# Kernel tuning notes

Hardware: AMD Instinct MI355X
Metric: run time of the kernel (lower is better)

The kernel has to match this reference:

```python
import jax, jax.numpy as jnp
import numpy as np

FACTOR = 5


def setup_inputs() -> dict:
    key = jax.random.key(0)
    k1, k2, k3, k4 = jax.random.split(key, 4)
    B, L, H, D = 4, 2048, 8, 64
    sample_k = min(FACTOR * int(np.ceil(np.log(L))), L)  # 40
    return {
        "query": jax.random.normal(k1, (B, L, H, D), dtype=jnp.float32),
        "key": jax.random.normal(k2, (B, L, H, D), dtype=jnp.float32),
        "value": jax.random.normal(k3, (B, L, H, D), dtype=jnp.float32),
        "index_sample": jax.random.randint(k4, (L, sample_k), 0, L, dtype=jnp.int32),
    }


def reference(query, key, value, index_sample):
    # query/key/value: (B, L, H, D); mask_flag=True, output_attention=False
    B, L_Q, H, D = query.shape
    L_K = key.shape[1]
    q = jnp.swapaxes(query, 1, 2)  # (B,H,L_Q,D)
    k = jnp.swapaxes(key, 1, 2)    # (B,H,L_K,D)
    v = jnp.swapaxes(value, 1, 2)  # (B,H,L_K,D)

    U_part = min(FACTOR * int(np.ceil(np.log(L_K))), L_K)  # sample_k
    u = min(FACTOR * int(np.ceil(np.log(L_Q))), L_Q)       # n_top

    # --- _prob_QK: sampled QK scores, sparsity measure M, top-u queries ---
    # K_sample: gather sample_k keys per query position -> (B,H,L_Q,sample_k,D)
    K_sample = k[:, :, index_sample, :]
    Q_K_sample = jnp.einsum("bhid,bhisd->bhis", q, K_sample)  # (B,H,L_Q,sample_k)
    M = Q_K_sample.max(axis=-1) - Q_K_sample.sum(axis=-1) / L_K  # (B,H,L_Q)
    _, M_top = jax.lax.top_k(M, u)  # (B,H,u) indices of selected queries

    Q_reduce = jnp.take_along_axis(q, M_top[..., None], axis=2)  # (B,H,u,D)
    scores = jnp.einsum("bhud,bhkd->bhuk", Q_reduce, k)          # (B,H,u,L_K)

    scale = 1.0 / jnp.sqrt(jnp.float32(D))
    scores = scores * scale

    # --- initial context: causal cumsum of V (mask_flag=True) ---
    context = jnp.cumsum(v, axis=2)  # (B,H,L_Q,D)

    # --- update context: causal ProbMask on selected rows, softmax, scatter ---
    # mask[b,h,t,kk] = kk > M_top[b,h,t]
    mask = jnp.arange(L_K)[None, None, None, :] > M_top[..., None]
    scores = jnp.where(mask, -jnp.inf, scores)
    attn = jax.nn.softmax(scores, axis=-1)
    ctx_upd = jnp.einsum("bhuk,bhkd->bhud", attn, v)  # (B,H,u,D)

    b_idx = jnp.arange(context.shape[0])[:, None, None]
    h_idx = jnp.arange(context.shape[1])[None, :, None]
    context = context.at[b_idx, h_idx, M_top].set(ctx_upd)

    return jnp.swapaxes(context, 1, 2)  # (B, L_Q, H, D)
```

## Files before the change

kernel.cpp:

```cpp
#include <hip/hip_runtime.h>
#include <hip/hip_bf16.h>
#include <math.h>

constexpr int B = 4;
constexpr int L = 2048;
constexpr int H = 8;
constexpr int D = 64;
constexpr int S = 40;
constexpr int U = 40;
constexpr int C = 32;
constexpr int CHUNK = L / C;
constexpr int NSEG = 16;
constexpr int SEG  = L / NSEG;
constexpr int PAH  = 688;

__global__ void fused_Mpart(const float* __restrict__ q,
                            const float* __restrict__ k,
                            const float* __restrict__ v,
                            const int*   __restrict__ samp,
                            float* __restrict__ M,
                            float* __restrict__ part) {
    __shared__ float pa[H * PAH];
    int tid = threadIdx.x;

    if (blockIdx.x < 256) {
        int idx = blockIdx.x * 256 + tid;
        int b   = idx >> 14;
        int rem = idx & 16383;
        int c   = rem >> 9;
        int hd  = rem & 511;
        const float* base = v + ((size_t)(b * L + c * CHUNK) * H * D) + hd;
        float s = 0.f;
        for (int i = 0; i < CHUNK; i++) s += base[(size_t)i * (H * D)];
        int h = hd >> 6, d = hd & 63;
        part[((size_t)(b * H + h) * C + c) * D + d] = s;
        return;
    }

    int blk = blockIdx.x - 256;
    int xcd = blk & 7;
    int b   = xcd >> 1;
    int l   = ((blk >> 3) << 1) | (xcd & 1);
    int h      = tid >> 5;
    int lane32 = tid & 31;
    int g  = lane32 >> 4;
    int d4 = lane32 & 15;

    const float4 qv = *(const float4*)(q + ((size_t)(b * L + l) * H + h) * D + d4 * 4);
    const int* srow = samp + l * S;
    float* pah = pa + h * PAH;

#pragma unroll 10
    for (int sb = 0; sb < S; sb += 2) {
        int i0 = srow[sb];
        int i1 = srow[sb + 1];
        int idx = g ? i1 : i0;
        int s = sb + g;
        float4 kv = *(const float4*)(k + ((size_t)(b * L + idx) * H + h) * D + d4 * 4);
        pah[s * 17 + d4] = qv.x * kv.x + qv.y * kv.y + qv.z * kv.z + qv.w * kv.w;
    }
    __syncthreads();

    int s1 = lane32;
    float t0 = 0.f, t1 = 0.f, t2 = 0.f, t3 = 0.f;
#pragma unroll
    for (int i = 0; i < 16; i += 4) {
        t0 += pah[s1 * 17 + i];
        t1 += pah[s1 * 17 + i + 1];
        t2 += pah[s1 * 17 + i + 2];
        t3 += pah[s1 * 17 + i + 3];
    }
    float dot1 = (t0 + t1) + (t2 + t3);
    float mv = dot1, sv = dot1;
    if (lane32 < S - 32) {
        int s2 = 32 + lane32;
        float u0 = 0.f, u1 = 0.f, u2 = 0.f, u3 = 0.f;
#pragma unroll
        for (int i = 0; i < 16; i += 4) {
            u0 += pah[s2 * 17 + i];
            u1 += pah[s2 * 17 + i + 1];
            u2 += pah[s2 * 17 + i + 2];
            u3 += pah[s2 * 17 + i + 3];
        }
        float dot2 = (u0 + u1) + (u2 + u3);
        mv = fmaxf(mv, dot2);
        sv += dot2;
    }
#pragma unroll
    for (int off = 1; off <= 16; off <<= 1) {
        mv = fmaxf(mv, __shfl_xor(mv, off));
        sv += __shfl_xor(sv, off);
    }
    if (lane32 == 0) M[(size_t)(b * H + h) * L + l] = mv - sv * (1.0f / (float)L);
}

__global__ void fused_topk_cumsum(const float* __restrict__ M,
                                  const float* __restrict__ v,
                                  const float* __restrict__ part,
                                  int* __restrict__ Mtop,
                                  float* __restrict__ out) {
    int tid = threadIdx.x;

    if (blockIdx.x >= 32) {
        int idx = (blockIdx.x - 32) * 64 + tid;
        int b   = idx >> 14;
        int rem = idx & 16383;
        int c   = rem >> 9;
        int hd  = rem & 511;
        int h = hd >> 6, d = hd & 63;

        float run = 0.f;
        for (int cc = 0; cc < c; cc++)
            run += part[((size_t)(b * H + h) * C + cc) * D + d];

        const float* base  = v   + ((size_t)(b * L + c * CHUNK) * H * D) + hd;
        float*       obase = out + ((size_t)(b * L + c * CHUNK) * H * D) + hd;
        for (int i = 0; i < CHUNK; i++) {
            run += base[(size_t)i * (H * D)];
            obase[(size_t)i * (H * D)] = run;
        }
        return;
    }

    int bh   = blockIdx.x;
    int base = tid * 32;
    const float* row = M + (size_t)bh * L;

    unsigned int vals[32];
#pragma unroll
    for (int r4 = 0; r4 < 8; r4++) {
        float4 f = *(const float4*)(row + base + r4 * 4);
        const float ff[4] = {f.x, f.y, f.z, f.w};
#pragma unroll
        for (int j = 0; j < 4; j++) {
            unsigned int i = __float_as_uint(ff[j]);
            vals[r4 * 4 + j] = (i & 0x80000000u) ? ~i : (i | 0x80000000u);
        }
    }

    unsigned long long k1 = 0ull, k2 = 0ull;
#pragma unroll
    for (int r = 0; r < 32; r++) {
        unsigned long long kk =
            ((unsigned long long)vals[r] << 32) | (unsigned int)~(base + r);
        if (kk > k1) { k2 = k1; k1 = kk; }
        else if (kk > k2) { k2 = kk; }
    }

    for (int it = 0; it < U; it += 2) {
        unsigned long long a1 = k1, a2 = k2;
#pragma unroll
        for (int off = 1; off < 64; off <<= 1) {
            unsigned long long o1 = __shfl_xor(a1, off);
            unsigned long long o2 = __shfl_xor(a2, off);
            unsigned long long hi = a1 > o1 ? a1 : o1;
            unsigned long long lo = a1 > o1 ? o1 : a1;
            unsigned long long ss = a2 > o2 ? a2 : o2;
            a1 = hi;
            a2 = lo > ss ? lo : ss;
        }
        int i1 = (int)~(unsigned int)a1;
        int i2 = (int)~(unsigned int)a2;
        if (tid == 0) {
            Mtop[bh * U + it]     = i1;
            Mtop[bh * U + it + 1] = i2;
        }
        bool own1 = (i1 >> 5) == tid;
        bool own2 = (i2 >> 5) == tid;
        if (own1 | own2) {
            int r1 = own1 ? (i1 & 31) : 32;
            int r2 = own2 ? (i2 & 31) : 32;
#pragma unroll
            for (int r = 0; r < 32; r++)
                if (r == r1 || r == r2) vals[r] = 0u;
            k1 = 0ull; k2 = 0ull;
#pragma unroll
            for (int r = 0; r < 32; r++) {
                unsigned long long kk =
                    ((unsigned long long)vals[r] << 32) | (unsigned int)~(base + r);
                if (kk > k1) { k2 = k1; k1 = kk; }
                else if (kk > k2) { k2 = kk; }
            }
        }
    }
}

__global__ __launch_bounds__(256, 2)
void attn_batched(const float* __restrict__ q,
                  const float* __restrict__ k,
                  const float* __restrict__ v,
                  const int*   __restrict__ Mtop,
                  float* __restrict__ ml,
                  float* __restrict__ pacc) {
    int blk = blockIdx.x;
    int xcd = blk & 7;
    int b   = xcd >> 1;
    int r   = ((blk >> 3) << 1) | (xcd & 1);
    int h   = r >> 4;
    int seg = r & 15;
    int bh  = b * H + h;
    int j0  = seg * SEG;
    int tid = threadIdx.x;

    __shared__ float Qs[U * D];
    __shared__ float KV[SEG * D];
    __shared__ float Sc[U * SEG];
    __shared__ float red[U * 4];
    __shared__ float mrow[U];
    __shared__ int   qis[U];

    if (tid < U) qis[tid] = Mtop[bh * U + tid];
    __syncthreads();

    for (int i = tid; i < U * 16; i += 256) {
        int u = i >> 4, d4 = i & 15;
        *(float4*)&Qs[u * D + d4 * 4] =
            *(const float4*)(q + ((size_t)(b * L + qis[u]) * H + h) * D + d4 * 4);
    }
    for (int i = tid; i < SEG * 16; i += 256) {
        int rr = i >> 4, d4 = i & 15;
        float4 kv = *(const float4*)(k + ((size_t)(b * L + j0 + rr) * H + h) * D + d4 * 4);
        *(float4*)&KV[rr * D + (d4 ^ (rr & 15)) * 4] = kv;
    }
    __syncthreads();

    int ug = tid >> 5;
    int jg = tid & 31;
    int jlow = jg & 15;
    float acc[5][4];
#pragma unroll
    for (int uu = 0; uu < 5; uu++)
#pragma unroll
        for (int jj = 0; jj < 4; jj++) acc[uu][jj] = 0.f;

#pragma unroll
    for (int kk4 = 0; kk4 < 16; kk4++) {
        float4 kf[4];
        int slot = kk4 ^ jlow;
#pragma unroll
        for (int jj = 0; jj < 4; jj++)
            kf[jj] = *(const float4*)&KV[(jg + 32 * jj) * D + slot * 4];
#pragma unroll
        for (int uu = 0; uu < 5; uu++) {
            float4 qf = *(const float4*)&Qs[(ug * 5 + uu) * D + kk4 * 4];
#pragma unroll
            for (int jj = 0; jj < 4; jj++) {
                acc[uu][jj] += qf.x * kf[jj].x + qf.y * kf[jj].y
                             + qf.z * kf[jj].z + qf.w * kf[jj].w;
            }
        }
    }
#pragma unroll
    for (int uu = 0; uu < 5; uu++) {
        int u = ug * 5 + uu;
        int um = u & 15;
#pragma unroll
        for (int jj = 0; jj < 4; jj++) {
            int j = jg + 32 * jj;
            Sc[u * SEG + 4 * ((j >> 2) ^ um) + (j & 3)] = acc[uu][jj] * 0.125f;
        }
    }
    __syncthreads();

    for (int i = tid; i < SEG * 16; i += 256) {
        int rr = i >> 4, d4 = i & 15;
        float4 vv = *(const float4*)(v + ((size_t)(b * L + j0 + rr) * H + h) * D + d4 * 4);
        *(float4*)&KV[rr * D + (d4 ^ (rr & 15)) * 4] = vv;
    }

    int su = tid >> 2, sq = tid & 3;
    int nkc = 0;
    if (tid < U * 4) {
        int nk = qis[su] + 1 - j0;
        nkc = nk < 0 ? 0 : (nk > SEG ? SEG : nk);
        int um = su & 15;
        float mvx = -INFINITY;
        for (int t = 0; t < 32; t++) {
            int i = sq + 4 * t;
            if (i < nkc) mvx = fmaxf(mvx, Sc[su * SEG + 4 * ((i >> 2) ^ um) + (i & 3)]);
        }
        red[su * 4 + sq] = mvx;
    }
    __syncthreads();
    if (tid < U) {
        float m = fmaxf(fmaxf(red[tid * 4], red[tid * 4 + 1]),
                        fmaxf(red[tid * 4 + 2], red[tid * 4 + 3]));
        mrow[tid] = m;
    }
    __syncthreads();
    if (tid < U * 4) {
        float m = mrow[su];
        int um = su & 15;
        float ls = 0.f;
        for (int t = 0; t < 32; t++) {
            int i = sq + 4 * t;
            int addr = su * SEG + 4 * ((i >> 2) ^ um) + (i & 3);
            float e = 0.f;
            if (i < nkc) e = __expf(Sc[addr] - m);
            Sc[addr] = e;
            ls += e;
        }
        red[su * 4 + sq] = ls;
    }
    __syncthreads();
    if (tid < U) {
        float ls = (red[tid * 4] + red[tid * 4 + 1]) + (red[tid * 4 + 2] + red[tid * 4 + 3]);
        size_t mli = 2 * ((size_t)(bh * U + tid) * NSEG + seg);
        ml[mli]     = mrow[tid];
        ml[mli + 1] = ls;
    }

    int vg = jg;
    float a2[5][2];
#pragma unroll
    for (int uu = 0; uu < 5; uu++) { a2[uu][0] = 0.f; a2[uu][1] = 0.f; }

    for (int j4 = 0; j4 < 32; j4++) {
        float4 pf[5];
#pragma unroll
        for (int uu = 0; uu < 5; uu++) {
            int u = ug * 5 + uu;
            pf[uu] = *(const float4*)&Sc[u * SEG + 4 * (j4 ^ (u & 15))];
        }
#pragma unroll
        for (int jj = 0; jj < 4; jj++) {
            int j = j4 * 4 + jj;
            int fo = 4 * ((vg >> 1) ^ (j & 15)) + ((2 * vg) & 3);
            float2 vv = *(const float2*)&KV[j * D + fo];
#pragma unroll
            for (int uu = 0; uu < 5; uu++) {
                float p = ((const float*)&pf[uu])[jj];
                a2[uu][0] += p * vv.x;
                a2[uu][1] += p * vv.y;
            }
        }
    }
#pragma unroll
    for (int uu = 0; uu < 5; uu++) {
        int u = ug * 5 + uu;
        float2 w2 = make_float2(a2[uu][0], a2[uu][1]);
        *(float2*)&pacc[((size_t)(bh * U + u) * NSEG + seg) * D + 2 * vg] = w2;
    }
}

__global__ void attn_combine(const int* __restrict__ Mtop,
                             const float* __restrict__ ml,
                             const float* __restrict__ pacc,
                             float* __restrict__ out) {
    int row = blockIdx.x * 4 + (threadIdx.x >> 6);
    int u  = row % U;
    int bh = row / U;
    int h  = bh % H;
    int b  = bh / H;
    int d  = threadIdx.x & 63;
    int qi = Mtop[bh * U + u];

    size_t r0 = (size_t)row * NSEG;
    float m = -INFINITY;
#pragma unroll
    for (int s = 0; s < NSEG; s++) m = fmaxf(m, ml[2 * (r0 + s)]);

    float lt = 0.f, acc = 0.f;
#pragma unroll
    for (int s = 0; s < NSEG; s++) {
        float ms = ml[2 * (r0 + s)];
        float w  = __expf(ms - m);
        lt  += ml[2 * (r0 + s) + 1] * w;
        acc += pacc[(r0 + s) * D + d] * w;
    }
    out[((size_t)(b * L + qi) * H + h) * D + d] = acc / lt;
}

extern "C" void kernel_launch(void* const* d_in, const int* in_sizes, int n_in,
                              void* d_out, int out_size, void* d_ws, size_t ws_size,
                              hipStream_t stream) {
    const float* q    = (const float*)d_in[0];
    const float* k    = (const float*)d_in[1];
    const float* v    = (const float*)d_in[2];
    const int*   samp = (const int*)d_in[3];
    float* out = (float*)d_out;

    float* M    = (float*)d_ws;
    int*   Mtop = (int*)(M + (size_t)B * H * L);
    float* part = (float*)(Mtop + (size_t)B * H * U);
    float* ml   = part + (size_t)B * H * C * D;
    float* pacc = ml + (size_t)B * H * U * NSEG * 2;

    fused_Mpart<<<256 + B * L, 256, 0, stream>>>(q, k, v, samp, M, part);
    fused_topk_cumsum<<<32 + 1024, 64, 0, stream>>>(M, v, part, Mtop, out);
    attn_batched<<<B * H * NSEG, 256, 0, stream>>>(q, k, v, Mtop, ml, pacc);
    attn_combine<<<B * H * U / 4, 256, 0, stream>>>(Mtop, ml, pacc, out);
}
```

Baseline: 184.4 us.

## Replace iterative warp top-k with radix-select histogram threshold and compaction

```diff
diff --git a/kernel.cpp b/kernel.cpp
--- a/kernel.cpp
+++ b/kernel.cpp
@@ -122,65 +122,106 @@
         return;
     }
 
+    __shared__ unsigned hist[16 * 256];
+    __shared__ unsigned selS[2];
+
     int bh   = blockIdx.x;
-    int base = tid * 32;
+    int lane = tid;
+    int base = lane * 32;
     const float* row = M + (size_t)bh * L;
 
-    unsigned int vals[32];
+    unsigned vals[32];
 #pragma unroll
     for (int r4 = 0; r4 < 8; r4++) {
         float4 f = *(const float4*)(row + base + r4 * 4);
         const float ff[4] = {f.x, f.y, f.z, f.w};
 #pragma unroll
         for (int j = 0; j < 4; j++) {
-            unsigned int i = __float_as_uint(ff[j]);
+            unsigned i = __float_as_uint(ff[j]);
             vals[r4 * 4 + j] = (i & 0x80000000u) ? ~i : (i | 0x80000000u);
         }
     }
 
-    unsigned long long k1 = 0ull, k2 = 0ull;
+    unsigned prefix = 0;
+    unsigned R = U;
+#pragma unroll
+    for (int p = 0; p < 4; p++) {
+        int sh = 24 - 8 * p;
+        {
+            uint4* h4 = (uint4*)hist;
+#pragma unroll
+            for (int i = 0; i < 16; i++) {
+                h4[lane + i * 64] = make_uint4(0u, 0u, 0u, 0u);
+            }
+        }
+        __syncthreads();
+        unsigned pbase = (lane & 15) * 256;
+#pragma unroll
+        for (int r = 0; r < 32; r++) {
+            unsigned vv = vals[r];
+            bool match = (p == 0) || ((vv >> (sh + 8)) == prefix);
+            if (match) atomicAdd(&hist[pbase + ((vv >> sh) & 255u)], 1u);
+        }
+        __syncthreads();
+        int b0 = lane * 4;
+        unsigned c0 = 0, c1 = 0, c2 = 0, c3 = 0;
+#pragma unroll
+        for (int pp = 0; pp < 16; pp++) {
+            const unsigned* hp = &hist[pp * 256 + b0];
+            c0 += hp[0]; c1 += hp[1]; c2 += hp[2]; c3 += hp[3];
+        }
+        unsigned t = c0 + c1 + c2 + c3;
+        unsigned s = t;
+#pragma unroll
+        for (int off = 1; off < 64; off <<= 1) {
+            unsigned n = __shfl_down(s, off);
+            if (lane + off < 64) s += n;
+        }
+        unsigned Sx = s - t;
+        unsigned suf3 = Sx;
+        unsigned suf2 = Sx + c3;
+        unsigned suf1 = Sx + c3 + c2;
+        unsigned suf0 = Sx + c3 + c2 + c1;
+        if (suf0 < R && R <= suf0 + c0) { selS[0] = b0;     selS[1] = R - suf0; }
+        if (suf1 < R && R <= suf1 + c1) { selS[0] = b0 + 1; selS[1] = R - suf1; }
+        if (suf2 < R && R <= suf2 + c2) { selS[0] = b0 + 2; selS[1] = R - suf2; }
+        if (suf3 < R && R <= suf3 + c3) { selS[0] = b0 + 3; selS[1] = R - suf3; }
+        __syncthreads();
+        prefix = (prefix << 8) | selS[0];
+        R = selS[1];
+        __syncthreads();
+    }
+    unsigned vstar = prefix;
+    unsigned Rstar = R;
+    unsigned n1 = U - Rstar;
+
+    unsigned cgt = 0, ceq = 0;
 #pragma unroll
     for (int r = 0; r < 32; r++) {
-        unsigned long long kk =
-            ((unsigned long long)vals[r] << 32) | (unsigned int)~(base + r);
-        if (kk > k1) { k2 = k1; k1 = kk; }
-        else if (kk > k2) { k2 = kk; }
-    }
-
-    for (int it = 0; it < U; it += 2) {
-        unsigned long long a1 = k1, a2 = k2;
-#pragma unroll
-        for (int off = 1; off < 64; off <<= 1) {
-            unsigned long long o1 = __shfl_xor(a1, off);
-            unsigned long long o2 = __shfl_xor(a2, off);
-            unsigned long long hi = a1 > o1 ? a1 : o1;
-            unsigned long long lo = a1 > o1 ? o1 : a1;
-            unsigned long long ss = a2 > o2 ? a2 : o2;
-            a1 = hi;
-            a2 = lo > ss ? lo : ss;
-        }
-        int i1 = (int)~(unsigned int)a1;
-        int i2 = (int)~(unsigned int)a2;
-        if (tid == 0) {
-            Mtop[bh * U + it]     = i1;
-            Mtop[bh * U + it + 1] = i2;
-        }
-        bool own1 = (i1 >> 5) == tid;
-        bool own2 = (i2 >> 5) == tid;
-        if (own1 | own2) {
-            int r1 = own1 ? (i1 & 31) : 32;
-            int r2 = own2 ? (i2 & 31) : 32;
-#pragma unroll
-            for (int r = 0; r < 32; r++)
-                if (r == r1 || r == r2) vals[r] = 0u;
-            k1 = 0ull; k2 = 0ull;
-#pragma unroll
-            for (int r = 0; r < 32; r++) {
-                unsigned long long kk =
-                    ((unsigned long long)vals[r] << 32) | (unsigned int)~(base + r);
-                if (kk > k1) { k2 = k1; k1 = kk; }
-                else if (kk > k2) { k2 = kk; }
-            }
+        cgt += (vals[r] > vstar) ? 1u : 0u;
+        ceq += (vals[r] == vstar) ? 1u : 0u;
+    }
+    unsigned ig = cgt, iq = ceq;
+#pragma unroll
+    for (int off = 1; off < 64; off <<= 1) {
+        unsigned ng = __shfl_up(ig, off);
+        unsigned nq = __shfl_up(iq, off);
+        if (lane >= off) { ig += ng; iq += nq; }
+    }
+    unsigned goff = ig - cgt;
+    unsigned toff = iq - ceq;
+    int p1 = (int)goff;
+    int pt = (int)(n1 + toff);
+    unsigned kk = 0;
+#pragma unroll
+    for (int r = 0; r < 32; r++) {
+        unsigned vv = vals[r];
+        if (vv > vstar) {
+            Mtop[bh * U + p1] = base + r;
+            p1++;
+        } else if (vv == vstar) {
+            if (toff + kk < Rstar) { Mtop[bh * U + pt] = base + r; pt++; }
+            kk++;
         }
     }
 }
```

New measurement: 158.5 us. 1.16x faster.
